# Kernel tuning notes

Hardware: AMD Instinct MI355X
Metric: run time of the kernel (lower is better)

Reference implementation:

```python
import jax, jax.numpy as jnp
import numpy as np

SIZES = [4096, 12288, 20480, 20480, 8192]  # atoms of degree 0..4 (atoms sorted by degree)
N_ATOMS = sum(SIZES)
BATCH = 1024
N_TASKS, N_CLASSES = 12, 2
BN_EPS = 1e-3  # keras BatchNormalization default epsilon


def setup_inputs() -> dict:
    key = jax.random.key(0)
    ks = jax.random.split(key, 20)
    inp = {}
    inp["atom_features"] = jax.random.normal(ks[0], (N_ATOMS, 75), jnp.float32)
    starts = np.concatenate([[0], np.cumsum(SIZES)[:-1]])
    inp["degree_slice"] = jnp.asarray(np.stack([starts, np.array(SIZES)], 1), jnp.int32)
    inp["membership"] = jax.random.randint(ks[1], (N_ATOMS,), 0, BATCH, jnp.int32)
    inp["n_samples"] = BATCH
    for d in range(1, 5):
        inp[f"deg_adj_{d}"] = jax.random.randint(ks[1 + d], (SIZES[d], d), 0, N_ATOMS, jnp.int32)

    def w(k, shape, s=0.05):
        return s * jax.random.normal(k, shape, jnp.float32)

    # GraphConv weights: order [relW_deg1, selfW_deg1, ..., relW_deg4, selfW_deg4, selfW_deg0]
    inp["gc1_W"] = w(ks[6], (9, 75, 256)); inp["gc1_b"] = w(ks[7], (9, 256))
    inp["gc2_W"] = w(ks[8], (9, 256, 256)); inp["gc2_b"] = w(ks[9], (9, 256))

    def bn_params(k, c):  # rows: gamma, beta, moving_mean, moving_var
        g = 1.0 + 0.1 * jax.random.normal(k, (c,), jnp.float32)
        b = 0.1 * jax.random.normal(jax.random.fold_in(k, 1), (c,), jnp.float32)
        return jnp.stack([g, b, jnp.zeros((c,), jnp.float32), jnp.ones((c,), jnp.float32)])

    inp["bn1"] = bn_params(ks[10], 256)
    inp["bn2"] = bn_params(ks[11], 256)
    inp["bn3"] = bn_params(ks[12], 512)
    inp["dense_W"] = w(ks[13], (256, 512)); inp["dense_b"] = w(ks[14], (512,))
    inp["head_W"] = w(ks[15], (2 * 512, N_TASKS * N_CLASSES)); inp["head_b"] = w(ks[16], (N_TASKS * N_CLASSES,))
    return inp


def _graph_conv(x, adjs, W, b):
    # degree-0 atoms: self transform only (last weight matrix)
    pieces = [x[: SIZES[0]] @ W[8] + b[8]]
    off = SIZES[0]
    for d in range(1, 5):
        nd = SIZES[d]
        self_atoms = x[off: off + nd]
        rel = jnp.take(x, adjs[d - 1], axis=0).sum(axis=1)  # [nd, F] neighbor sum
        out = rel @ W[2 * (d - 1)] + b[2 * (d - 1)] + self_atoms @ W[2 * d - 1] + b[2 * d - 1]
        pieces.append(out)
        off += nd
    return jax.nn.relu(jnp.concatenate(pieces, axis=0))


def _graph_pool(x, adjs):
    pieces = [x[: SIZES[0]]]  # degree-0: passthrough
    off = SIZES[0]
    for d in range(1, 5):
        nd = SIZES[d]
        self_atoms = x[off: off + nd]
        neigh = jnp.take(x, adjs[d - 1], axis=0)  # [nd, d, F]
        pieces.append(jnp.maximum(self_atoms, neigh.max(axis=1)))
        off += nd
    return jnp.concatenate(pieces, axis=0)


def _bn(x, p):  # inference batchnorm with moving stats
    g, b, m, v = p
    return g * (x - m) * jax.lax.rsqrt(v + BN_EPS) + b


def reference(atom_features, degree_slice, membership, n_samples,
              deg_adj_1, deg_adj_2, deg_adj_3, deg_adj_4,
              gc1_W, gc1_b, gc2_W, gc2_b, bn1, bn2, bn3,
              dense_W, dense_b, head_W, head_b):
    adjs = (deg_adj_1, deg_adj_2, deg_adj_3, deg_adj_4)
    x = atom_features
    for W, b, bn in ((gc1_W, gc1_b, bn1), (gc2_W, gc2_b, bn2)):
        x = _bn(_graph_conv(x, adjs, W, b), bn)
        x = _graph_pool(x, adjs)
    h = _bn(jax.nn.relu(x @ dense_W + dense_b), bn3)  # [N_ATOMS, 512]
    # GraphGather: per-molecule sum and max, tanh activation
    seg_sum = jax.ops.segment_sum(h, membership, num_segments=BATCH)
    seg_max = jax.ops.segment_max(h, membership, num_segments=BATCH)
    fp = jnp.tanh(jnp.concatenate([seg_sum, seg_max], axis=1))  # neural fingerprint [BATCH, 1024]
    logits = (fp @ head_W + head_b).reshape(BATCH, N_TASKS, N_CLASSES)[: int(n_samples)]  # trim
    return jax.nn.softmax(logits, axis=-1), logits, fp
```

## Files before the change

### kernel.cpp

```cpp
#include <hip/hip_runtime.h>
#include <hip/hip_bf16.h>
#include <math.h>

#define NA 65536
#define MAXSEG 160

typedef _Float16 half8 __attribute__((ext_vector_type(8)));
typedef _Float16 h4    __attribute__((ext_vector_type(4)));
typedef float float4v  __attribute__((ext_vector_type(4)));

typedef __attribute__((address_space(3))) unsigned int lds_uint;
typedef __attribute__((address_space(1))) const unsigned int g_uint;

__device__ __forceinline__ void async16(const void* g, void* l) {
    __builtin_amdgcn_global_load_lds((g_uint*)g, (lds_uint*)l, 16, 0, 0);
}


__device__ __forceinline__ int unperm128(int p) {
    return (p & ~127) + (((p & 127) & 7) << 4) + ((p & 127) >> 3);
}

__device__ __forceinline__ unsigned mapf(float x) {
    unsigned b = __float_as_uint(x);
    return (b & 0x80000000u) ? ~b : (b | 0x80000000u);
}
#define MAPF_NEGINF 0x007FFFFFu

__device__ __forceinline__ void atom_seg(int atom, int& d, int& loc,
                                         const int* a1, const int* a2,
                                         const int* a3, const int* a4,
                                         const int*& adj) {
    if (atom < 4096)       { d = 0; loc = 0; adj = nullptr; }
    else if (atom < 16384) { d = 1; adj = a1; loc = atom - 4096; }
    else if (atom < 36864) { d = 2; adj = a2; loc = atom - 16384; }
    else if (atom < 57344) { d = 3; adj = a3; loc = atom - 36864; }
    else                   { d = 4; adj = a4; loc = atom - 57344; }
}

__global__ __launch_bounds__(256) void prep_kernel(
    const float* __restrict__ af,
    const float* __restrict__ gc1W, const float* __restrict__ gc1b,
    const float* __restrict__ gc2W, const float* __restrict__ gc2b,
    const float* __restrict__ dW, const float* __restrict__ hW,
    _Float16* __restrict__ af16, _Float16* __restrict__ Wc1, float* __restrict__ bias1,
    _Float16* __restrict__ Wc2, float* __restrict__ bias2,
    _Float16* __restrict__ dWt, float* __restrict__ hWt, int* __restrict__ count,
    float* __restrict__ fpsum, unsigned* __restrict__ fpmaxu) {
    int b = blockIdx.x, t = threadIdx.x;
    if (b < 5120) {
        int idx = b * 256 + t;
        int atom = idx / 20, k4 = idx - atom * 20;
        int c0 = k4 * 4;
        h4 o;
        #pragma unroll
        for (int j = 0; j < 4; j++) {
            int c = c0 + j;
            o[j] = (_Float16)((c < 75) ? af[(size_t)atom * 75 + c] : 0.f);
        }
        *(h4*)(af16 + (size_t)atom * 80 + c0) = o;
    } else if (b < 5920) {
        int idx = (b - 5120) * 256 + t;
        if (idx < 204800) {
            int k = idx % 160, n = (idx / 160) & 255, seg = idx / (160 * 256);
            float v = 0.f;
            if (k < 80) {
                if (k < 75) { int w = (seg == 0) ? 8 : (2 * seg - 1); v = gc1W[(w * 75 + k) * 256 + n]; }
            } else {
                int kk = k - 80;
                if (kk < 75 && seg > 0) { int w = 2 * (seg - 1); v = gc1W[(w * 75 + kk) * 256 + n]; }
            }
            Wc1[(size_t)(seg * 256 + n) * 160 + k] = (_Float16)v;
        }
        if (idx < 1280) {
            int n = idx & 255, seg = idx >> 8;
            bias1[idx] = (seg == 0) ? gc1b[8 * 256 + n]
                                    : gc1b[(2 * seg - 1) * 256 + n] + gc1b[2 * (seg - 1) * 256 + n];
        }
    } else if (b < 8480) {
        int idx = (b - 5920) * 256 + t;
        int k = idx & 511, n = (idx >> 9) & 255, seg = idx >> 17;
        float v = 0.f;
        if (k < 256) {
            int w = (seg == 0) ? 8 : (2 * seg - 1);
            v = gc2W[(w * 256 + unperm128(k)) * 256 + n];
        } else if (seg > 0) {
            int w = 2 * (seg - 1);
            v = gc2W[(w * 256 + unperm128(k - 256)) * 256 + n];
        }
        Wc2[(size_t)(seg * 256 + n) * 512 + k] = (_Float16)v;
        if (idx < 1280) {
            int nn = idx & 255, sg = idx >> 8;
            bias2[idx] = (sg == 0) ? gc2b[8 * 256 + nn]
                                   : gc2b[(2 * sg - 1) * 256 + nn] + gc2b[2 * (sg - 1) * 256 + nn];
        }
    } else if (b < 8992) {
        int idx = (b - 8480) * 256 + t;
        int n = idx >> 8, k = idx & 255;
        dWt[(size_t)n * 256 + k] = (_Float16)dW[(size_t)unperm128(k) * 512 + n];
    } else if (b < 9088) {
        int idx = (b - 8992) * 256 + t;
        int o = idx / 1024, k = idx & 1023;
        hWt[idx] = hW[k * 24 + o];
    } else if (b < 9092) {
        int i = (b - 9088) * 256 + t;
        if (i < 1024) count[i] = 0;
    } else if (b < 11140) {
        fpsum[(size_t)(b - 9092) * 256 + t] = 0.f;
    } else {
        fpmaxu[(size_t)(b - 11140) * 256 + t] = MAPF_NEGINF;
    }
}

__global__ void bucket_kernel(const int* __restrict__ mem, int* __restrict__ count,
                              int* __restrict__ list) {
    int i = blockIdx.x * 256 + threadIdx.x;
    int seg = mem[i];
    int pos = atomicAdd(&count[seg], 1);
    if (pos < MAXSEG) list[seg * MAXSEG + pos] = i;
}

__global__ __launch_bounds__(1024) void scan_kernel(const int* __restrict__ count,
                                                    int* __restrict__ offs) {
    __shared__ int tmp[1024];
    int t = threadIdx.x;
    int v = count[t]; if (v > MAXSEG) v = MAXSEG;
    tmp[t] = v;
    __syncthreads();
    for (int off = 1; off < 1024; off <<= 1) {
        int x = (t >= off) ? tmp[t - off] : 0;
        __syncthreads();
        tmp[t] += x;
        __syncthreads();
    }
    offs[t] = tmp[t] - v;
}

__global__ __launch_bounds__(256) void build_sorted_kernel(
    const int* __restrict__ count, const int* __restrict__ offs,
    const int* __restrict__ list, int* __restrict__ sorted) {
    int seg = blockIdx.x;
    int n = count[seg]; if (n > MAXSEG) n = MAXSEG;
    int base = offs[seg];
    for (int i = threadIdx.x; i < n; i += 256)
        sorted[base + i] = list[seg * MAXSEG + i] | (seg << 16);
}

__global__ __launch_bounds__(256) void gather1n_kernel(
    const _Float16* __restrict__ af16,
    const int* __restrict__ a1, const int* __restrict__ a2,
    const int* __restrict__ a3, const int* __restrict__ a4,
    _Float16* __restrict__ Xn1) {
    int idx = blockIdx.x * 256 + threadIdx.x;
    int atom = idx / 20, k4 = idx - atom * 20;
    int c0 = k4 * 4;
    int d, loc; const int* adj;
    atom_seg(atom, d, loc, a1, a2, a3, a4, adj);
    float s0 = 0.f, s1 = 0.f, s2 = 0.f, s3 = 0.f;
    for (int j = 0; j < d; j++) {
        int nb = adj[(size_t)loc * d + j];
        h4 v = *(const h4*)(af16 + (size_t)nb * 80 + c0);
        s0 += (float)v[0]; s1 += (float)v[1]; s2 += (float)v[2]; s3 += (float)v[3];
    }
    h4 o; o[0] = (_Float16)s0; o[1] = (_Float16)s1; o[2] = (_Float16)s2; o[3] = (_Float16)s3;
    *(h4*)(Xn1 + (size_t)atom * 80 + c0) = o;
}

__global__ __launch_bounds__(256) void gather2n_kernel(
    const _Float16* __restrict__ p,
    const int* __restrict__ a1, const int* __restrict__ a2,
    const int* __restrict__ a3, const int* __restrict__ a4,
    _Float16* __restrict__ Xn) {
    int atom = blockIdx.x * 8 + (threadIdx.x >> 5);
    int l = threadIdx.x & 31;
    int d, loc; const int* adj;
    atom_seg(atom, d, loc, a1, a2, a3, a4, adj);
    float s[8] = {};
    for (int j = 0; j < d; j++) {
        int nb = adj[(size_t)loc * d + j];
        half8 v = *(const half8*)(p + (size_t)nb * 256 + l * 8);
        #pragma unroll
        for (int e = 0; e < 8; e++) s[e] += (float)v[e];
    }
    half8 o;
    #pragma unroll
    for (int e = 0; e < 8; e++) o[e] = (_Float16)s[e];
    *(half8*)(Xn + (size_t)atom * 256 + l * 8) = o;
}

template<int K, int N, int BK, int SB>
__global__ __launch_bounds__(256) void gemm_kernel(
    const _Float16* __restrict__ X, const _Float16* __restrict__ Xn,
    const _Float16* __restrict__ Wt,
    const float* __restrict__ bias, const float* __restrict__ bnp,
    int wstride, int bstride, _Float16* __restrict__ out) {
    constexpr int NC8 = BK / 8;
    constexpr int MASK = NC8 - 1;
    __shared__ __align__(16) _Float16 As[128 * BK];
    __shared__ __align__(16) _Float16 Bs[128 * BK];
    constexpr int nb = N / 128;
    int G = gridDim.x;
    int bid = (blockIdx.x & 7) * (G >> 3) + (blockIdx.x >> 3);
    int m0 = (bid / nb) * 128, n0 = (bid % nb) * 128;
    int t = m0 >> 7;
    int seg = (t < 32) ? 0 : (t < 128) ? 1 : (t < 288) ? 2 : (t < 448) ? 3 : 4;
    const _Float16* Wb = Wt + (size_t)seg * wstride;
    const float* bia = bias + seg * bstride;
    int tid = threadIdx.x, lane = tid & 63, wave = tid >> 6;
    int wm = (wave >> 1) * 64, wn = (wave & 1) * 64;
    int lrow = lane & 15, lq = lane >> 4;
    float4v acc[4][4] = {};
    for (int kc = 0; kc < K / BK; kc++) {
        #pragma unroll
        for (int q = 0; q < NC8 / 2; q++) {
            int slot = q * 256 + wave * 64 + lane;
            int row = slot / NC8;
            int cs = slot & MASK;
            int c8 = cs ^ (row & MASK);
            const _Float16* gA;
            if (SB == 0) {
                gA = X + (size_t)(m0 + row) * K + kc * BK + c8 * 8;
            } else {
                int kcol = kc * BK + c8 * 8;
                gA = (kcol < SB) ? X  + (size_t)(m0 + row) * SB + kcol
                                 : Xn + (size_t)(m0 + row) * SB + (kcol - SB);
            }
            async16(gA, As + (size_t)(q * 256 + wave * 64) * 8);
            const _Float16* gB = Wb + (size_t)(n0 + row) * K + kc * BK + c8 * 8;
            async16(gB, Bs + (size_t)(q * 256 + wave * 64) * 8);
        }
        __syncthreads();
        #pragma unroll
        for (int kl = 0; kl < BK / 32; kl++) {
            half8 af[4], bf[4];
            #pragma unroll
            for (int i = 0; i < 4; i++) {
                int ra = wm + i * 16 + lrow;
                int ca = (kl * 4 + lq) ^ (ra & MASK);
                af[i] = *(const half8*)(As + ra * BK + ca * 8);
                int rb = wn + i * 16 + lrow;
                int cb = (kl * 4 + lq) ^ (rb & MASK);
                bf[i] = *(const half8*)(Bs + rb * BK + cb * 8);
            }
            #pragma unroll
            for (int mi = 0; mi < 4; mi++)
                #pragma unroll
                for (int ni = 0; ni < 4; ni++)
                    acc[mi][ni] = __builtin_amdgcn_mfma_f32_16x16x32_f16(af[mi], bf[ni], acc[mi][ni], 0, 0, 0);
        }
        __syncthreads();
    }
    float bv[4], sc[4], mn[4], be[4];
    #pragma unroll
    for (int ni = 0; ni < 4; ni++) {
        int c = n0 + wn + ni * 16 + lrow;
        bv[ni] = bia[c];
        float g = bnp[c], vr = bnp[3 * N + c];
        mn[ni] = bnp[2 * N + c]; be[ni] = bnp[N + c];
        sc[ni] = g * rsqrtf(vr + 1e-3f);
    }
    int p0 = n0 + lrow * 8 + (wave & 1) * 4;
    #pragma unroll
    for (int mi = 0; mi < 4; mi++) {
        #pragma unroll
        for (int r = 0; r < 4; r++) {
            h4 pack;
            #pragma unroll
            for (int ni = 0; ni < 4; ni++) {
                float v = acc[mi][ni][r] + bv[ni];
                v = fmaxf(v, 0.f);
                v = sc[ni] * (v - mn[ni]) + be[ni];
                pack[ni] = (_Float16)v;
            }
            int row = m0 + wm + mi * 16 + lq * 4 + r;
            *(h4*)(out + (size_t)row * N + p0) = pack;
        }
    }
}

__global__ __launch_bounds__(256) void pool_f16_kernel(
    const _Float16* __restrict__ x,
    const int* __restrict__ a1, const int* __restrict__ a2,
    const int* __restrict__ a3, const int* __restrict__ a4,
    _Float16* __restrict__ out) {
    int atom = blockIdx.x * 8 + (threadIdx.x >> 5);
    int l = threadIdx.x & 31;
    int d, loc; const int* adj;
    atom_seg(atom, d, loc, a1, a2, a3, a4, adj);
    half8 m = *(const half8*)(x + (size_t)atom * 256 + l * 8);
    float mv[8];
    #pragma unroll
    for (int e = 0; e < 8; e++) mv[e] = (float)m[e];
    for (int j = 0; j < d; j++) {
        int nb = adj[(size_t)loc * d + j];
        half8 v = *(const half8*)(x + (size_t)nb * 256 + l * 8);
        #pragma unroll
        for (int e = 0; e < 8; e++) mv[e] = fmaxf(mv[e], (float)v[e]);
    }
    half8 o;
    #pragma unroll
    for (int e = 0; e < 8; e++) o[e] = (_Float16)mv[e];
    *(half8*)(out + (size_t)atom * 256 + l * 8) = o;
}

__global__ __launch_bounds__(256) void dense_kernel(
    const _Float16* __restrict__ X, const _Float16* __restrict__ Wt,
    const float* __restrict__ bias, const float* __restrict__ bnp,
    const int* __restrict__ sorted,
    float* __restrict__ fpsum, unsigned* __restrict__ fpmaxu) {
    constexpr int NBINS = 8;
    __shared__ __align__(16) _Float16 As[128 * 64];
    __shared__ __align__(16) _Float16 Bs[128 * 64];
    __shared__ float binsum[NBINS * 128];
    __shared__ unsigned binmax[NBINS * 128];
    __shared__ int spk[128];
    int G = gridDim.x;
    int bid = (blockIdx.x & 7) * (G >> 3) + (blockIdx.x >> 3);
    int m0 = (bid >> 2) * 128, n0 = (bid & 3) * 128;
    int tid = threadIdx.x, lane = tid & 63, wave = tid >> 6;
    if (tid < 128) spk[tid] = sorted[m0 + tid];
    for (int e = tid; e < NBINS * 128; e += 256) { binsum[e] = 0.f; binmax[e] = MAPF_NEGINF; }
    __syncthreads();
    const _Float16* baseA[4]; const _Float16* baseB[4];
    #pragma unroll
    for (int q = 0; q < 4; q++) {
        int slot = q * 256 + wave * 64 + lane;
        int row = slot >> 3, cs = slot & 7, c8 = cs ^ (row & 7);
        baseA[q] = X + (size_t)(spk[row] & 0xFFFF) * 256 + c8 * 8;
        baseB[q] = Wt + (size_t)(n0 + row) * 256 + c8 * 8;
    }
    int wm = (wave >> 1) * 64, wn = (wave & 1) * 64;
    int lrow = lane & 15, lq = lane >> 4;
    float4v acc[4][4] = {};
    for (int kc = 0; kc < 4; kc++) {
        #pragma unroll
        for (int q = 0; q < 4; q++) {
            async16(baseA[q] + kc * 64, As + (size_t)(q * 256 + wave * 64) * 8);
            async16(baseB[q] + kc * 64, Bs + (size_t)(q * 256 + wave * 64) * 8);
        }
        __syncthreads();
        #pragma unroll
        for (int kl = 0; kl < 2; kl++) {
            half8 af[4], bf[4];
            #pragma unroll
            for (int i = 0; i < 4; i++) {
                int ra = wm + i * 16 + lrow;
                int ca = (kl * 4 + lq) ^ (ra & 7);
                af[i] = *(const half8*)(As + ra * 64 + ca * 8);
                int rb = wn + i * 16 + lrow;
                int cb = (kl * 4 + lq) ^ (rb & 7);
                bf[i] = *(const half8*)(Bs + rb * 64 + cb * 8);
            }
            #pragma unroll
            for (int mi = 0; mi < 4; mi++)
                #pragma unroll
                for (int ni = 0; ni < 4; ni++)
                    acc[mi][ni] = __builtin_amdgcn_mfma_f32_16x16x32_f16(af[mi], bf[ni], acc[mi][ni], 0, 0, 0);
        }
        __syncthreads();
    }
    float bv[4], sc[4], mn[4], be[4];
    #pragma unroll
    for (int ni = 0; ni < 4; ni++) {
        int c = n0 + wn + ni * 16 + lrow;
        bv[ni] = bias[c];
        float g = bnp[c], vr = bnp[3 * 512 + c];
        mn[ni] = bnp[2 * 512 + c]; be[ni] = bnp[512 + c];
        sc[ni] = g * rsqrtf(vr + 1e-3f);
    }
    int pcol = lrow * 8 + (wave & 1) * 4;
    int segbase = spk[0] >> 16;
    #pragma unroll
    for (int mi = 0; mi < 4; mi++) {
        int r0 = wm + mi * 16;
        int sFirst = spk[r0] >> 16, sLast = spk[r0 + 15] >> 16;
        if (sFirst == sLast) {
            int srel = sFirst - segbase; if (srel > NBINS - 1) srel = NBINS - 1;
            float ps[4], pm[4];
            #pragma unroll
            for (int ni = 0; ni < 4; ni++) { ps[ni] = 0.f; pm[ni] = -INFINITY; }
            #pragma unroll
            for (int r = 0; r < 4; r++) {
                #pragma unroll
                for (int ni = 0; ni < 4; ni++) {
                    float v = acc[mi][ni][r] + bv[ni];
                    v = fmaxf(v, 0.f);
                    v = sc[ni] * (v - mn[ni]) + be[ni];
                    ps[ni] += v;
                    pm[ni] = fmaxf(pm[ni], v);
                }
            }
            #pragma unroll
            for (int ni = 0; ni < 4; ni++) {
                ps[ni] += __shfl_xor(ps[ni], 16, 64);
                ps[ni] += __shfl_xor(ps[ni], 32, 64);
                pm[ni] = fmaxf(pm[ni], __shfl_xor(pm[ni], 16, 64));
                pm[ni] = fmaxf(pm[ni], __shfl_xor(pm[ni], 32, 64));
            }
            if (lq == 0) {
                int bb = srel * 128 + pcol;
                #pragma unroll
                for (int ni = 0; ni < 4; ni++) {
                    atomicAdd(&binsum[bb + ni], ps[ni]);
                    atomicMax(&binmax[bb + ni], mapf(pm[ni]));
                }
            }
        } else {
            int curs = -1;
            float ps[4], pm[4];
            #pragma unroll
            for (int r = 0; r < 4; r++) {
                int row = r0 + lq * 4 + r;
                int srel = (spk[row] >> 16) - segbase;
                if (srel > NBINS - 1) srel = NBINS - 1;
                if (srel != curs) {
                    if (curs >= 0) {
                        int bb = curs * 128 + pcol;
                        #pragma unroll
                        for (int ni = 0; ni < 4; ni++) {
                            atomicAdd(&binsum[bb + ni], ps[ni]);
                            atomicMax(&binmax[bb + ni], mapf(pm[ni]));
                        }
                    }
                    curs = srel;
                    #pragma unroll
                    for (int ni = 0; ni < 4; ni++) { ps[ni] = 0.f; pm[ni] = -INFINITY; }
                }
                #pragma unroll
                for (int ni = 0; ni < 4; ni++) {
                    float v = acc[mi][ni][r] + bv[ni];
                    v = fmaxf(v, 0.f);
                    v = sc[ni] * (v - mn[ni]) + be[ni];
                    ps[ni] += v;
                    pm[ni] = fmaxf(pm[ni], v);
                }
            }
            {
                int bb = curs * 128 + pcol;
                #pragma unroll
                for (int ni = 0; ni < 4; ni++) {
                    atomicAdd(&binsum[bb + ni], ps[ni]);
                    atomicMax(&binmax[bb + ni], mapf(pm[ni]));
                }
            }
        }
    }
    __syncthreads();
    int nseg = (spk[127] >> 16) - segbase + 1;
    if (nseg > NBINS) nseg = NBINS;
    for (int e = tid; e < nseg * 128; e += 256) {
        int s = e >> 7, pc = e & 127;
        float v = binsum[e];
        if (v != 0.f) atomicAdd(&fpsum[(size_t)(segbase + s) * 512 + n0 + pc], v);
        unsigned u = binmax[e];
        if (u != MAPF_NEGINF) atomicMax(&fpmaxu[(size_t)(segbase + s) * 512 + n0 + pc], u);
    }
}

__global__ __launch_bounds__(256) void head_kernel(
    const float* __restrict__ fpsum, const unsigned* __restrict__ fpmaxu,
    const float* __restrict__ hWt, const float* __restrict__ hb,
    float* __restrict__ fp, float* __restrict__ logits, float* __restrict__ probs) {
    __shared__ float fps[1024];
    __shared__ float red[32];
    int s = blockIdx.x;
    for (int i = threadIdx.x; i < 512; i += 256) {
        float sv = tanhf(fpsum[(size_t)s * 512 + i]);
        unsigned u = fpmaxu[(size_t)s * 512 + i];
        unsigned b = (u & 0x80000000u) ? (u & 0x7FFFFFFFu) : ~u;
        float mv = tanhf(__uint_as_float(b));
        int chan = unperm128(i);
        fps[chan] = sv; fps[512 + chan] = mv;
        fp[(size_t)s * 1024 + chan] = sv;
        fp[(size_t)s * 1024 + 512 + chan] = mv;
    }
    __syncthreads();
    int t = threadIdx.x;
    int o = t >> 3, kp = t & 7;
    float acc = 0.f;
    if (o < 24) {
        const float* w = hWt + (size_t)o * 1024 + kp * 128;
        const float* f = fps + kp * 128;
        #pragma unroll 8
        for (int i = 0; i < 128; i++) acc = fmaf(f[i], w[i], acc);
    }
    acc += __shfl_down(acc, 4, 64);
    acc += __shfl_down(acc, 2, 64);
    acc += __shfl_down(acc, 1, 64);
    if (o < 24 && kp == 0) red[o] = acc + hb[o];
    __syncthreads();
    if (t < 24) {
        float a = red[t];
        float an = red[t ^ 1];
        logits[(size_t)s * 24 + t] = a;
        probs[(size_t)s * 24 + t] = 1.f / (1.f + expf(an - a));
    }
}

extern "C" void kernel_launch(void* const* d_in, const int* in_sizes, int n_in,
                              void* d_out, int out_size, void* d_ws, size_t ws_size,
                              hipStream_t stream) {
    const float* af         = (const float*)d_in[0];
    const int*   membership = (const int*)d_in[2];
    const int*   a1 = (const int*)d_in[4];
    const int*   a2 = (const int*)d_in[5];
    const int*   a3 = (const int*)d_in[6];
    const int*   a4 = (const int*)d_in[7];
    const float* gc1W = (const float*)d_in[8];
    const float* gc1b = (const float*)d_in[9];
    const float* gc2W = (const float*)d_in[10];
    const float* gc2b = (const float*)d_in[11];
    const float* bn1  = (const float*)d_in[12];
    const float* bn2  = (const float*)d_in[13];
    const float* bn3  = (const float*)d_in[14];
    const float* dW   = (const float*)d_in[15];
    const float* db   = (const float*)d_in[16];
    const float* hW   = (const float*)d_in[17];
    const float* hb   = (const float*)d_in[18];

    float* out    = (float*)d_out;
    float* probs  = out;
    float* logits = out + 24576;
    float* fp     = out + 49152;

    _Float16* Wc1  = (_Float16*)d_ws;
    _Float16* Wc2  = Wc1 + 204800;
    _Float16* dWt  = Wc2 + 655360;
    float* bias1   = (float*)(dWt + 131072);
    float* bias2   = bias1 + 1280;
    float* hWt     = bias2 + 1280;
    float* fpsum   = hWt + 24576;
    unsigned* fpmaxu = (unsigned*)(fpsum + 524288);
    int* count     = (int*)(fpmaxu + 524288);
    int* offs      = count + 1024;
    int* sorted    = offs + 1024;
    int* list      = sorted + 65536;
    _Float16* bufSm  = (_Float16*)(list + 163840);
    _Float16* Xn     = bufSm + (size_t)NA * 160;
    _Float16* bufY   = Xn + (size_t)NA * 256;
    _Float16* bufP   = bufY + (size_t)NA * 256;
    _Float16* af16 = bufSm;
    _Float16* Xn1  = bufSm + (size_t)NA * 80;

    prep_kernel<<<13188, 256, 0, stream>>>(af, gc1W, gc1b, gc2W, gc2b, dW, hW,
                                           af16, Wc1, bias1, Wc2, bias2, dWt, hWt,
                                           count, fpsum, fpmaxu);
    bucket_kernel<<<256, 256, 0, stream>>>(membership, count, list);
    scan_kernel<<<1, 1024, 0, stream>>>(count, offs);
    build_sorted_kernel<<<1024, 256, 0, stream>>>(count, offs, list, sorted);
    gather1n_kernel<<<5120, 256, 0, stream>>>(af16, a1, a2, a3, a4, Xn1);
    gemm_kernel<160, 256, 32, 80><<<1024, 256, 0, stream>>>(af16, Xn1, Wc1, bias1, bn1,
                                                            256 * 160, 256, bufY);
    pool_f16_kernel<<<8192, 256, 0, stream>>>(bufY, a1, a2, a3, a4, bufP);
    gather2n_kernel<<<8192, 256, 0, stream>>>(bufP, a1, a2, a3, a4, Xn);
    gemm_kernel<512, 256, 64, 256><<<1024, 256, 0, stream>>>(bufP, Xn, Wc2, bias2, bn2,
                                                             256 * 512, 256, bufY);
    pool_f16_kernel<<<8192, 256, 0, stream>>>(bufY, a1, a2, a3, a4, bufP);
    dense_kernel<<<2048, 256, 0, stream>>>(bufP, dWt, db, bn3, sorted, fpsum, fpmaxu);
    head_kernel<<<1024, 256, 0, stream>>>(fpsum, fpmaxu, hWt, hb, fp, logits, probs);
}
```

Measured before the change: 307.6 us.

## Replace global atomics in segment reduction with per-tile partials reduced in head

```diff
diff --git a/kernel.cpp b/kernel.cpp
--- a/kernel.cpp
+++ b/kernel.cpp
@@ -45,8 +45,7 @@
     const float* __restrict__ dW, const float* __restrict__ hW,
     _Float16* __restrict__ af16, _Float16* __restrict__ Wc1, float* __restrict__ bias1,
     _Float16* __restrict__ Wc2, float* __restrict__ bias2,
-    _Float16* __restrict__ dWt, float* __restrict__ hWt, int* __restrict__ count,
-    float* __restrict__ fpsum, unsigned* __restrict__ fpmaxu) {
+    _Float16* __restrict__ dWt, float* __restrict__ hWt, int* __restrict__ count) {
     int b = blockIdx.x, t = threadIdx.x;
     if (b < 5120) {
         int idx = b * 256 + t;
@@ -102,13 +101,9 @@
         int idx = (b - 8992) * 256 + t;
         int o = idx / 1024, k = idx & 1023;
         hWt[idx] = hW[k * 24 + o];
-    } else if (b < 9092) {
+    } else {
         int i = (b - 9088) * 256 + t;
         if (i < 1024) count[i] = 0;
-    } else if (b < 11140) {
-        fpsum[(size_t)(b - 9092) * 256 + t] = 0.f;
-    } else {
-        fpmaxu[(size_t)(b - 11140) * 256 + t] = MAPF_NEGINF;
     }
 }
 
@@ -307,7 +302,7 @@
     const _Float16* __restrict__ X, const _Float16* __restrict__ Wt,
     const float* __restrict__ bias, const float* __restrict__ bnp,
     const int* __restrict__ sorted,
-    float* __restrict__ fpsum, unsigned* __restrict__ fpmaxu) {
+    float* __restrict__ psum, unsigned* __restrict__ pmax) {
     constexpr int NBINS = 8;
     __shared__ __align__(16) _Float16 As[128 * 64];
     __shared__ __align__(16) _Float16 Bs[128 * 64];
@@ -448,34 +443,64 @@
     __syncthreads();
     int nseg = (spk[127] >> 16) - segbase + 1;
     if (nseg > NBINS) nseg = NBINS;
+    int tile = m0 >> 7;
     for (int e = tid; e < nseg * 128; e += 256) {
         int s = e >> 7, pc = e & 127;
-        float v = binsum[e];
-        if (v != 0.f) atomicAdd(&fpsum[(size_t)(segbase + s) * 512 + n0 + pc], v);
-        unsigned u = binmax[e];
-        if (u != MAPF_NEGINF) atomicMax(&fpmaxu[(size_t)(segbase + s) * 512 + n0 + pc], u);
+        size_t slot = ((size_t)(tile * NBINS + s)) * 512 + n0 + pc;
+        psum[slot] = binsum[e];
+        pmax[slot] = binmax[e];
     }
 }
 
 __global__ __launch_bounds__(256) void head_kernel(
-    const float* __restrict__ fpsum, const unsigned* __restrict__ fpmaxu,
+    const float* __restrict__ psum, const unsigned* __restrict__ pmax,
+    const int* __restrict__ count, const int* __restrict__ offs,
+    const int* __restrict__ sorted,
     const float* __restrict__ hWt, const float* __restrict__ hb,
     float* __restrict__ fp, float* __restrict__ logits, float* __restrict__ probs) {
+    constexpr int NBINS = 8;
     __shared__ float fps[1024];
     __shared__ float red[32];
     int s = blockIdx.x;
-    for (int i = threadIdx.x; i < 512; i += 256) {
-        float sv = tanhf(fpsum[(size_t)s * 512 + i]);
-        unsigned u = fpmaxu[(size_t)s * 512 + i];
-        unsigned b = (u & 0x80000000u) ? (u & 0x7FFFFFFFu) : ~u;
+    int t = threadIdx.x;
+    int cnt = count[s]; if (cnt > MAXSEG) cnt = MAXSEG;
+    int off = offs[s];
+    float sum0 = 0.f, sum1 = 0.f;
+    unsigned mu0 = MAPF_NEGINF, mu1 = MAPF_NEGINF;
+    if (cnt > 0) {
+        int t0 = off >> 7, t1 = (off + cnt - 1) >> 7;
+        for (int tt = t0; tt <= t1; tt++) {
+            int segbase_t = sorted[tt << 7] >> 16;
+            int srel = s - segbase_t;
+            if (srel < 0) srel = 0;
+            if (srel > NBINS - 1) srel = NBINS - 1;
+            const float* ps = psum + ((size_t)(tt * NBINS + srel)) * 512;
+            const unsigned* pm = pmax + ((size_t)(tt * NBINS + srel)) * 512;
+            sum0 += ps[t]; sum1 += ps[t + 256];
+            unsigned a0 = pm[t], a1 = pm[t + 256];
+            mu0 = (a0 > mu0) ? a0 : mu0;
+            mu1 = (a1 > mu1) ? a1 : mu1;
+        }
+    }
+    {
+        float sv = tanhf(sum0);
+        unsigned b = (mu0 & 0x80000000u) ? (mu0 & 0x7FFFFFFFu) : ~mu0;
         float mv = tanhf(__uint_as_float(b));
-        int chan = unperm128(i);
+        int chan = unperm128(t);
         fps[chan] = sv; fps[512 + chan] = mv;
         fp[(size_t)s * 1024 + chan] = sv;
         fp[(size_t)s * 1024 + 512 + chan] = mv;
     }
+    {
+        float sv = tanhf(sum1);
+        unsigned b = (mu1 & 0x80000000u) ? (mu1 & 0x7FFFFFFFu) : ~mu1;
+        float mv = tanhf(__uint_as_float(b));
+        int chan = unperm128(t + 256);
+        fps[chan] = sv; fps[512 + chan] = mv;
+        fp[(size_t)s * 1024 + chan] = sv;
+        fp[(size_t)s * 1024 + 512 + chan] = mv;
+    }
     __syncthreads();
-    int t = threadIdx.x;
     int o = t >> 3, kp = t & 7;
     float acc = 0.f;
     if (o < 24) {
@@ -529,9 +554,9 @@
     float* bias1   = (float*)(dWt + 131072);
     float* bias2   = bias1 + 1280;
     float* hWt     = bias2 + 1280;
-    float* fpsum   = hWt + 24576;
-    unsigned* fpmaxu = (unsigned*)(fpsum + 524288);
-    int* count     = (int*)(fpmaxu + 524288);
+    float* psum    = hWt + 24576;
+    unsigned* pmax = (unsigned*)(psum + 2097152);
+    int* count     = (int*)(pmax + 2097152);
     int* offs      = count + 1024;
     int* sorted    = offs + 1024;
     int* list      = sorted + 65536;
@@ -542,9 +567,8 @@
     _Float16* af16 = bufSm;
     _Float16* Xn1  = bufSm + (size_t)NA * 80;
 
-    prep_kernel<<<13188, 256, 0, stream>>>(af, gc1W, gc1b, gc2W, gc2b, dW, hW,
-                                           af16, Wc1, bias1, Wc2, bias2, dWt, hWt,
-                                           count, fpsum, fpmaxu);
+    prep_kernel<<<9092, 256, 0, stream>>>(af, gc1W, gc1b, gc2W, gc2b, dW, hW,
+                                          af16, Wc1, bias1, Wc2, bias2, dWt, hWt, count);
     bucket_kernel<<<256, 256, 0, stream>>>(membership, count, list);
     scan_kernel<<<1, 1024, 0, stream>>>(count, offs);
     build_sorted_kernel<<<1024, 256, 0, stream>>>(count, offs, list, sorted);
@@ -556,6 +580,7 @@
     gemm_kernel<512, 256, 64, 256><<<1024, 256, 0, stream>>>(bufP, Xn, Wc2, bias2, bn2,
                                                              256 * 512, 256, bufY);
     pool_f16_kernel<<<8192, 256, 0, stream>>>(bufY, a1, a2, a3, a4, bufP);
-    dense_kernel<<<2048, 256, 0, stream>>>(bufP, dWt, db, bn3, sorted, fpsum, fpmaxu);
-    head_kernel<<<1024, 256, 0, stream>>>(fpsum, fpmaxu, hWt, hb, fp, logits, probs);
-}
+    dense_kernel<<<2048, 256, 0, stream>>>(bufP, dWt, db, bn3, sorted, psum, pmax);
+    head_kernel<<<1024, 256, 0, stream>>>(psum, pmax, count, offs, sorted,
+                                          hWt, hb, fp, logits, probs);
+}
```

Result: no change. 306.8 us (-0.3%).
